# Kernel optimization log

Measured on AMD Instinct MI355X. Metric: run time of the kernel, lower is better.

Reference implementation:

```python
import jax, jax.numpy as jnp
import numpy as np

B, T, C, H = 4, 2048, 1024, 16
D = C // H  # head dim = 64


def setup_inputs() -> dict:
    key = jax.random.key(0)
    ks = jax.random.split(key, 5)
    s = 1.0 / np.sqrt(C)
    return {
        "x": jax.random.normal(ks[0], (B, T, C), dtype=jnp.float32),
        "Wq": jax.random.normal(ks[1], (C, C), dtype=jnp.float32) * s,
        "bq": jnp.zeros((C,), dtype=jnp.float32),
        "Wk": jax.random.normal(ks[2], (C, C), dtype=jnp.float32) * s,
        "bk": jnp.zeros((C,), dtype=jnp.float32),
        "Wv": jax.random.normal(ks[3], (C, C), dtype=jnp.float32) * s,
        "bv": jnp.zeros((C,), dtype=jnp.float32),
        "Wp": jax.random.normal(ks[4], (C, C), dtype=jnp.float32) * s,
        "bp": jnp.zeros((C,), dtype=jnp.float32),
    }


def reference(x, Wq, bq, Wk, bk, Wv, bv, Wp, bp):
    Bb, Tt, Cc = x.shape
    # QKV projections (torch Linear: y = x @ W.T + b)
    q = (x @ Wq.T + bq).reshape(Bb, Tt, H, D).transpose(0, 2, 1, 3)  # [B,H,T,D]
    k = (x @ Wk.T + bk).reshape(Bb, Tt, H, D).transpose(0, 2, 1, 3)
    v = (x @ Wv.T + bv).reshape(Bb, Tt, H, D).transpose(0, 2, 1, 3)
    att = jnp.einsum("bhqd,bhkd->bhqk", q, k) / jnp.sqrt(jnp.float32(D))
    causal = jnp.tril(jnp.ones((Tt, Tt), dtype=bool))
    att = jnp.where(causal[None, None], att, -jnp.inf)
    att = jax.nn.softmax(att, axis=-1)
    y = jnp.einsum("bhqk,bhkd->bhqd", att, v)  # [B,H,T,D]
    y = y.transpose(0, 2, 1, 3).reshape(Bb, Tt, Cc)
    return y @ Wp.T + bp
```

## Files before the change

### kernel.cpp

```cpp
#include <hip/hip_runtime.h>

typedef unsigned short u16;
typedef unsigned int u32;

typedef __attribute__((ext_vector_type(4))) float f32x4;
typedef __attribute__((ext_vector_type(8))) short bf16x8;


__device__ inline u16 f2b(float f) {
  union { float f; u32 u; } x; x.f = f;
  u32 u = x.u;
  u32 r = (u + 0x7fffu + ((u >> 16) & 1u)) >> 16;
  return (u16)r;
}

__device__ inline u32 cvtpk(float lo, float hi) {
  u32 r;
  asm("v_cvt_pk_bf16_f32 %0, %1, %2" : "=v"(r) : "v"(lo), "v"(hi));
  return r;
}

__device__ inline void gload_lds16(const void* g, void* l) {
  __builtin_amdgcn_global_load_lds(
      (const __attribute__((address_space(1))) u32*)g,
      (__attribute__((address_space(3))) u32*)l, 16, 0, 0);
}


__global__ __launch_bounds__(256) void cvt_all(const float* __restrict__ x,
                                               const float* __restrict__ w0,
                                               const float* __restrict__ w1,
                                               const float* __restrict__ w2,
                                               const float* __restrict__ w3,
                                               u16* __restrict__ xs,
                                               u16* __restrict__ wsz,
                                               u16* __restrict__ wps) {
  int g = blockIdx.x * 256 + threadIdx.x;
  int grow = g >> 7;
  int c = g & 127;
  const float* src;
  char* dst;
  int row;
  if (grow < 8192) {
    row = grow;
    src = x + (size_t)row * 1024;
    dst = (char*)xs;
  } else if (grow < 11264) {
    row = grow - 8192;
    src = (row < 1024) ? w0 + (size_t)row * 1024
         : (row < 2048) ? w1 + (size_t)(row - 1024) * 1024
                        : w2 + (size_t)(row - 2048) * 1024;
    dst = (char*)wsz;
  } else {
    row = grow - 11264;
    src = w3 + (size_t)row * 1024;
    dst = (char*)wps;
  }
  int kt = c >> 3, cc = (c & 7) ^ (row & 7);
  float4 lo = *(const float4*)(src + c * 8);
  float4 hi = *(const float4*)(src + c * 8 + 4);
  union { u16 s[8]; uint4 v; } o;
  o.s[0] = f2b(lo.x); o.s[1] = f2b(lo.y); o.s[2] = f2b(lo.z); o.s[3] = f2b(lo.w);
  o.s[4] = f2b(hi.x); o.s[5] = f2b(hi.y); o.s[6] = f2b(hi.z); o.s[7] = f2b(hi.w);
  *(uint4*)(dst + (size_t)(row >> 8) * 524288 + kt * 32768 +
            (row & 255) * 128 + cc * 16) = o.v;
}


__global__ __launch_bounds__(512) void gemm_qkv(const u16* __restrict__ Aswz,
                                                const u16* __restrict__ Wswz,
                                                const float* __restrict__ bq,
                                                const float* __restrict__ bk,
                                                const float* __restrict__ bv,
                                                u16* __restrict__ outQ,
                                                u16* __restrict__ outK,
                                                u16* __restrict__ outVt,
                                                float qscale) {
  __shared__ u16 lds[3][24576];

  const int t = threadIdx.x;
  const int lane = t & 63;
  const int w = t >> 6;
  const int wm = w >> 1, wn = w & 1;
  const int lr = lane & 15, lg = lane >> 4;

  int bid = blockIdx.y * 24 + blockIdx.x;
  int swz = (bid & 7) * 96 + (bid >> 3);
  const int mBase = (swz / 24) * 256;
  const int nBase = (swz % 24) * 128;
  const int mode = nBase >> 10;
  const int noff = nBase & 255;

  const char* Ap = (const char*)Aswz + (size_t)(mBase >> 8) * 524288;
  const char* Bp = (const char*)Wswz + (size_t)(nBase >> 8) * 524288 +
                   noff * 128;

  f32x4 acc[4][4];
#pragma unroll
  for (int i = 0; i < 4; ++i)
#pragma unroll
    for (int j = 0; j < 4; ++j) acc[i][j] = (f32x4){0.f, 0.f, 0.f, 0.f};

  auto stage = [&](int buf, int kt2) {
    const char* As = Ap + (size_t)kt2 * 32768;
    const char* Bs = Bp + (size_t)kt2 * 32768;
    char* Ad = (char*)&lds[buf][0];
    char* Bd = (char*)&lds[buf][16384];
#pragma unroll
    for (int l = 0; l < 4; ++l)
      gload_lds16(As + (l * 512 + t) * 16, Ad + (l * 512 + t) * 16);
#pragma unroll
    for (int l = 0; l < 2; ++l)
      gload_lds16(Bs + (l * 512 + t) * 16, Bd + (l * 512 + t) * 16);
  };

  stage(0, 0);
  stage(1, 1);

  for (int kt = 0; kt < 16; ++kt) {
    if (kt < 15) asm volatile("s_waitcnt vmcnt(6)" ::: "memory");
    else         asm volatile("s_waitcnt vmcnt(0)" ::: "memory");
    __builtin_amdgcn_s_barrier();
    if (kt + 2 < 16) stage((kt + 2) % 3, kt + 2);

    const int cb = kt % 3;
    const char* Ab = (const char*)&lds[cb][0];
    const char* Bb = (const char*)&lds[cb][16384];

    bf16x8 af[4][2], bf[4][2];
#pragma unroll
    for (int i = 0; i < 4; ++i) {
      int row = wm * 64 + i * 16 + lr;
#pragma unroll
      for (int kk = 0; kk < 2; ++kk)
        af[i][kk] = *(const bf16x8*)(Ab + row * 128 +
                                     ((kk * 64 + lg * 16) ^ ((row & 7) << 4)));
    }
#pragma unroll
    for (int j = 0; j < 4; ++j) {
      int rn = wn * 64 + j * 16 + lr;
#pragma unroll
      for (int kk = 0; kk < 2; ++kk)
        bf[j][kk] = *(const bf16x8*)(Bb + rn * 128 +
                                     ((kk * 64 + lg * 16) ^ ((rn & 7) << 4)));
    }

    __builtin_amdgcn_s_setprio(1);
#pragma unroll
    for (int i = 0; i < 4; ++i)
#pragma unroll
      for (int j = 0; j < 4; ++j)
#pragma unroll
        for (int kk = 0; kk < 2; ++kk)
          acc[i][j] = __builtin_amdgcn_mfma_f32_16x16x32_bf16(
              af[i][kk], bf[j][kk], acc[i][j], 0, 0, 0);
    __builtin_amdgcn_s_setprio(0);
  }

#pragma unroll
  for (int i = 0; i < 4; ++i) {
    int row = mBase + wm * 64 + i * 16 + lg * 4;
    int b_ = row >> 11, tp = row & 2047;
#pragma unroll
    for (int j = 0; j < 4; ++j) {
      int col = nBase + wn * 64 + j * 16 + lr;
      int ncol = col & 1023;
      int h = ncol >> 6, dd = ncol & 63;
      size_t bhOff = (size_t)(b_ * 16 + h) * 262144;
      if (mode == 2) {
        float bv_ = bv[ncol];
        ushort4 o;
        o.x = f2b(acc[i][j][0] + bv_);
        o.y = f2b(acc[i][j][1] + bv_);
        o.z = f2b(acc[i][j][2] + bv_);
        o.w = f2b(acc[i][j][3] + bv_);
        *(ushort4*)((char*)outVt + bhOff + (tp >> 6) * 8192 + dd * 128 +
                    ((((tp & 63) >> 3) << 4) ^ ((dd & 7) << 4)) +
                    (tp & 7) * 2) = o;
      } else if (mode == 0) {
        float bv_ = bq[ncol];
#pragma unroll
        for (int r = 0; r < 4; ++r)
          outQ[(((size_t)(b_ * 16 + h) * 2048) + tp + r) * 64 + dd] =
              f2b((acc[i][j][r] + bv_) * qscale);
      } else {
        float bv_ = bk[ncol];
#pragma unroll
        for (int r = 0; r < 4; ++r) {
          int tt = tp + r;
          *(u16*)((char*)outK + bhOff + (tt >> 6) * 8192 + (tt & 63) * 128 +
                  (((dd >> 3) << 4) ^ ((tt & 7) << 4)) + (dd & 7) * 2) =
              f2b(acc[i][j][r] + bv_);
        }
      }
    }
  }
}


__global__ __launch_bounds__(512) void gemm_proj(const u16* __restrict__ Aswz,
                                                 const u16* __restrict__ Wswz,
                                                 const float* __restrict__ bias,
                                                 float* __restrict__ outF) {
  __shared__ u16 lds[3][24576];

  const int t = threadIdx.x;
  const int lane = t & 63;
  const int w = t >> 6;
  const int wm = w >> 1, wn = w & 1;
  const int lr = lane & 15, lg = lane >> 4;

  int bid = blockIdx.y * 8 + blockIdx.x;
  int swz = (bid & 7) * 32 + (bid >> 3);
  const int mBase = (swz >> 3) * 256;
  const int nBase = (swz & 7) * 128;

  const char* Ap = (const char*)Aswz + (size_t)(mBase >> 8) * 524288;
  const char* Bp = (const char*)Wswz + (size_t)(nBase >> 8) * 524288 +
                   (nBase & 255) * 128;

  f32x4 acc[4][4];
#pragma unroll
  for (int i = 0; i < 4; ++i)
#pragma unroll
    for (int j = 0; j < 4; ++j) acc[i][j] = (f32x4){0.f, 0.f, 0.f, 0.f};

  auto stage = [&](int buf, int kt2) {
    const char* As = Ap + (size_t)kt2 * 32768;
    const char* Bs = Bp + (size_t)kt2 * 32768;
    char* Ad = (char*)&lds[buf][0];
    char* Bd = (char*)&lds[buf][16384];
#pragma unroll
    for (int l = 0; l < 4; ++l)
      gload_lds16(As + (l * 512 + t) * 16, Ad + (l * 512 + t) * 16);
#pragma unroll
    for (int l = 0; l < 2; ++l)
      gload_lds16(Bs + (l * 512 + t) * 16, Bd + (l * 512 + t) * 16);
  };

  stage(0, 0);
  stage(1, 1);

  for (int kt = 0; kt < 16; ++kt) {
    if (kt < 15) asm volatile("s_waitcnt vmcnt(6)" ::: "memory");
    else         asm volatile("s_waitcnt vmcnt(0)" ::: "memory");
    __builtin_amdgcn_s_barrier();
    if (kt + 2 < 16) stage((kt + 2) % 3, kt + 2);

    const int cb = kt % 3;
    const char* Ab = (const char*)&lds[cb][0];
    const char* Bb = (const char*)&lds[cb][16384];

    bf16x8 af[4][2], bf[4][2];
#pragma unroll
    for (int i = 0; i < 4; ++i) {
      int row = wm * 64 + i * 16 + lr;
#pragma unroll
      for (int kk = 0; kk < 2; ++kk)
        af[i][kk] = *(const bf16x8*)(Ab + row * 128 +
                                     ((kk * 64 + lg * 16) ^ ((row & 7) << 4)));
    }
#pragma unroll
    for (int j = 0; j < 4; ++j) {
      int rn = wn * 64 + j * 16 + lr;
#pragma unroll
      for (int kk = 0; kk < 2; ++kk)
        bf[j][kk] = *(const bf16x8*)(Bb + rn * 128 +
                                     ((kk * 64 + lg * 16) ^ ((rn & 7) << 4)));
    }

    __builtin_amdgcn_s_setprio(1);
#pragma unroll
    for (int i = 0; i < 4; ++i)
#pragma unroll
      for (int j = 0; j < 4; ++j)
#pragma unroll
        for (int kk = 0; kk < 2; ++kk)
          acc[i][j] = __builtin_amdgcn_mfma_f32_16x16x32_bf16(
              af[i][kk], bf[j][kk], acc[i][j], 0, 0, 0);
    __builtin_amdgcn_s_setprio(0);
  }

#pragma unroll
  for (int i = 0; i < 4; ++i) {
    int row = mBase + wm * 64 + i * 16 + lg * 4;
#pragma unroll
    for (int j = 0; j < 4; ++j) {
      int col = nBase + wn * 64 + j * 16 + lr;
      float bv = bias[col];
#pragma unroll
      for (int r = 0; r < 4; ++r)
        outF[(size_t)(row + r) * 1024 + col] = acc[i][j][r] + bv;
    }
  }
}


__global__ __launch_bounds__(512) void attn_fwd(const u16* __restrict__ qg,
                                                const u16* __restrict__ kswz,
                                                const u16* __restrict__ vswz,
                                                u16* __restrict__ ypan) {
  __shared__ u16 sK[2][64 * 64];
  __shared__ u16 sVt[2][64 * 64];

  const int t = threadIdx.x;
  const int lane = t & 63;
  const int w = t >> 6;
  const int lr = lane & 15, lg = lane >> 4;
  const int xk = (lr & 7) << 4;

  int bid0 = blockIdx.y * 8 + blockIdx.x;
  int swzb = (bid0 & 7) * 64 + (bid0 >> 3);
  const int bh = swzb >> 3;
  const int pair = swzb & 7;

  const char* kgb = (const char*)kswz + (size_t)bh * 262144;
  const char* vgb = (const char*)vswz + (size_t)bh * 262144;
  const u16* qb = qg + (size_t)bh * 131072;

  gload_lds16(kgb + t * 16, (char*)&sK[0][0] + t * 16);
  gload_lds16(vgb + t * 16, (char*)&sVt[0][0] + t * 16);

  f32x4 zero = {0.f, 0.f, 0.f, 0.f};
  const int b = bh >> 4, h = bh & 15;
  int tc = 0;

  for (int half = 0; half < 2; ++half) {
    const int qt = half ? pair : 15 - pair;
    const int nkt = 2 * qt + 2;
    const int wq0 = qt * 128 + w * 16;
    const int qrow = wq0 + lr;

    bf16x8 qf[2];
#pragma unroll
    for (int kk = 0; kk < 2; ++kk)
      qf[kk] = *(const bf16x8*)(qb + (size_t)qrow * 64 + kk * 32 + lg * 8);

    f32x4 accO[4];
#pragma unroll
    for (int n = 0; n < 4; ++n) accO[n] = zero;
    float lrun = 0.f;

    for (int kt = 0; kt < nkt; ++kt, ++tc) {
      const int cur = tc & 1;
      __syncthreads();

      int nextT = (kt + 1 < nkt) ? kt + 1 : (half == 0 ? 0 : -1);
      if (nextT >= 0) {
        gload_lds16(kgb + nextT * 8192 + t * 16,
                    (char*)&sK[cur ^ 1][0] + t * 16);
        gload_lds16(vgb + nextT * 8192 + t * 16,
                    (char*)&sVt[cur ^ 1][0] + t * 16);
      }

      if (kt * 64 > wq0 + 15) continue;

      const char* kb_ = (const char*)&sK[cur][0];
      const char* vb_ = (const char*)&sVt[cur][0];

      f32x4 s[4];
      __builtin_amdgcn_s_setprio(1);
#pragma unroll
      for (int n = 0; n < 4; ++n) {
        f32x4 a = zero;
#pragma unroll
        for (int kk = 0; kk < 2; ++kk) {
          bf16x8 kf = *(const bf16x8*)(kb_ + (n * 16 + lr) * 128 +
                                       ((kk * 64 + lg * 16) ^ xk));
          a = __builtin_amdgcn_mfma_f32_16x16x32_bf16(kf, qf[kk], a, 0, 0, 0);
        }
        s[n] = a;
      }
      __builtin_amdgcn_s_setprio(0);

      if (kt * 64 + 63 > wq0) {
#pragma unroll
        for (int n = 0; n < 4; ++n) {
          int key0 = kt * 64 + n * 16 + lg * 4;
#pragma unroll
          for (int r = 0; r < 4; ++r)
            s[n][r] = (key0 + r <= qrow) ? s[n][r] : -1e30f;
        }
      }

      u32 pk[4][2];
#pragma unroll
      for (int n = 0; n < 4; ++n) {
        float p0 = exp2f(s[n][0] - 12.f);
        float p1 = exp2f(s[n][1] - 12.f);
        float p2 = exp2f(s[n][2] - 12.f);
        float p3 = exp2f(s[n][3] - 12.f);
        lrun += (p0 + p1) + (p2 + p3);
        pk[n][0] = cvtpk(p0, p1);
        pk[n][1] = cvtpk(p2, p3);
      }

      const bool hi = (lg >> 1) & 1;
#pragma unroll
      for (int kk = 0; kk < 2; ++kk) {
        u32 g[4];
#pragma unroll
        for (int r = 0; r < 4; ++r) {
          const int rh = r >> 1, rl = r & 1;
          u32 give = ((lg & 1) ^ rh) ? pk[2 * kk + 1][rl] : pk[2 * kk][rl];
          int srcLane = ((lg & 1) * 2 + ((lg >> 1) ^ rh)) * 16 + lr;
          g[r] = (u32)__shfl((int)give, srcLane);
        }
        union { u32 u[4]; bf16x8 v; } pu;
        pu.u[0] = hi ? g[2] : g[0];
        pu.u[1] = hi ? g[3] : g[1];
        pu.u[2] = hi ? g[0] : g[2];
        pu.u[3] = hi ? g[1] : g[3];
        bf16x8 pf = pu.v;
        __builtin_amdgcn_s_setprio(1);
#pragma unroll
        for (int n = 0; n < 4; ++n) {
          bf16x8 vf = *(const bf16x8*)(vb_ + (n * 16 + lr) * 128 +
                                       ((kk * 64 + lg * 16) ^ xk));
          accO[n] = __builtin_amdgcn_mfma_f32_16x16x32_bf16(pf, vf, accO[n], 0, 0, 0);
        }
        __builtin_amdgcn_s_setprio(0);
      }
    }

    lrun += __shfl_xor(lrun, 16);
    lrun += __shfl_xor(lrun, 32);

#pragma unroll
    for (int r = 0; r < 4; ++r) {
      float linv = 1.f / __shfl(lrun, lg * 4 + r);
      int row = b * 2048 + qt * 128 + w * 16 + lg * 4 + r;
      char* rp = (char*)ypan + (size_t)(row >> 8) * 524288 +
                 h * 32768 + (row & 255) * 128;
#pragma unroll
      for (int n = 0; n < 4; ++n) {
        int cl = n * 16 + lr;
        *(u16*)(rp + ((((cl >> 3) ^ (row & 7)) << 4)) + (cl & 7) * 2) =
            f2b(accO[n][r] * linv);
      }
    }
  }
}


extern "C" void kernel_launch(void* const* d_in, const int* in_sizes, int n_in,
                              void* d_out, int out_size, void* d_ws, size_t ws_size,
                              hipStream_t stream) {
  const float* x  = (const float*)d_in[0];
  const float* Wq = (const float*)d_in[1];
  const float* bq = (const float*)d_in[2];
  const float* Wk = (const float*)d_in[3];
  const float* bk = (const float*)d_in[4];
  const float* Wv = (const float*)d_in[5];
  const float* bv = (const float*)d_in[6];
  const float* Wp = (const float*)d_in[7];
  const float* bp = (const float*)d_in[8];
  float* out = (float*)d_out;

  char* ws = (char*)d_ws;
  u16* xb  = (u16*)(ws);
  u16* wqb = (u16*)(ws + (16u << 20));
  u16* wpb = (u16*)(ws + (22u << 20));
  u16* qb  = (u16*)(ws + (24u << 20));
  u16* kb  = (u16*)(ws + (40u << 20));
  u16* vtb = (u16*)(ws + (56u << 20));
  u16* yb  = (u16*)(ws + (72u << 20));

  const float SCL = 0.18033688011112042f;

  cvt_all<<<6144, 256, 0, stream>>>(x, Wq, Wk, Wv, Wp, xb, wqb, wpb);

  gemm_qkv<<<dim3(24, 32), 512, 0, stream>>>(xb, wqb, bq, bk, bv,
                                             qb, kb, vtb, SCL);

  attn_fwd<<<dim3(8, 64), 512, 0, stream>>>(qb, kb, vtb, yb);

  gemm_proj<<<dim3(8, 32), 512, 0, stream>>>(yb, wpb, bp, out);
}
```

Baseline: 175.9 us.

## Use 32x32 MFMA tiles and split paired query tiles across wave halves

The attention kernel switches from 16x16x32 to 32x32x16 bf16 MFMAs, so each wave handles 32 query rows instead of 16. The two paired query tiles now run concurrently, with waves 0-3 on the long tile and waves 4-7 on the short one, instead of one after the other. This reduces loop iterations, barriers and K/V reloads. The cost is that the short-tile waves sit idle through the later key tiles, accumulator register use grows, and the softmax permutation is redone with a single xor-32 shuffle.

```diff
diff --git a/kernel.cpp b/kernel.cpp
--- a/kernel.cpp
+++ b/kernel.cpp
@@ -4,6 +4,7 @@
 typedef unsigned int u32;
 
 typedef __attribute__((ext_vector_type(4))) float f32x4;
+typedef __attribute__((ext_vector_type(16))) float f32x16;
 typedef __attribute__((ext_vector_type(8))) short bf16x8;
 
 
@@ -306,8 +307,8 @@
   const int t = threadIdx.x;
   const int lane = t & 63;
   const int w = t >> 6;
-  const int lr = lane & 15, lg = lane >> 4;
-  const int xk = (lr & 7) << 4;
+  const int qc = lane & 31;
+  const int hi = lane >> 5;
 
   int bid0 = blockIdx.y * 8 + blockIdx.x;
   int swzb = (bid0 & 7) * 64 + (bid0 >> 3);
@@ -318,126 +319,125 @@
   const char* vgb = (const char*)vswz + (size_t)bh * 262144;
   const u16* qb = qg + (size_t)bh * 131072;
 
+  const int qt = (w < 4) ? (15 - pair) : pair;
+  const int wq0 = qt * 128 + (w & 3) * 32;
+  const int qrow = wq0 + qc;
+  const int nkt = 2 * (15 - pair) + 2;
+
+  bf16x8 qf[4];
+#pragma unroll
+  for (int s = 0; s < 4; ++s)
+    qf[s] = *(const bf16x8*)(qb + (size_t)qrow * 64 + s * 16 + hi * 8);
+
   gload_lds16(kgb + t * 16, (char*)&sK[0][0] + t * 16);
   gload_lds16(vgb + t * 16, (char*)&sVt[0][0] + t * 16);
 
-  f32x4 zero = {0.f, 0.f, 0.f, 0.f};
+  f32x16 accO[2];
+#pragma unroll
+  for (int d = 0; d < 2; ++d)
+#pragma unroll
+    for (int i = 0; i < 16; ++i) accO[d][i] = 0.f;
+  float lrun = 0.f;
+
   const int b = bh >> 4, h = bh & 15;
-  int tc = 0;
-
-  for (int half = 0; half < 2; ++half) {
-    const int qt = half ? pair : 15 - pair;
-    const int nkt = 2 * qt + 2;
-    const int wq0 = qt * 128 + w * 16;
-    const int qrow = wq0 + lr;
-
-    bf16x8 qf[2];
-#pragma unroll
-    for (int kk = 0; kk < 2; ++kk)
-      qf[kk] = *(const bf16x8*)(qb + (size_t)qrow * 64 + kk * 32 + lg * 8);
-
-    f32x4 accO[4];
-#pragma unroll
-    for (int n = 0; n < 4; ++n) accO[n] = zero;
-    float lrun = 0.f;
-
-    for (int kt = 0; kt < nkt; ++kt, ++tc) {
-      const int cur = tc & 1;
-      __syncthreads();
-
-      int nextT = (kt + 1 < nkt) ? kt + 1 : (half == 0 ? 0 : -1);
-      if (nextT >= 0) {
-        gload_lds16(kgb + nextT * 8192 + t * 16,
-                    (char*)&sK[cur ^ 1][0] + t * 16);
-        gload_lds16(vgb + nextT * 8192 + t * 16,
-                    (char*)&sVt[cur ^ 1][0] + t * 16);
+
+  for (int kt = 0; kt < nkt; ++kt) {
+    const int cur = kt & 1;
+    __syncthreads();
+
+    if (kt + 1 < nkt) {
+      gload_lds16(kgb + (kt + 1) * 8192 + t * 16,
+                  (char*)&sK[cur ^ 1][0] + t * 16);
+      gload_lds16(vgb + (kt + 1) * 8192 + t * 16,
+                  (char*)&sVt[cur ^ 1][0] + t * 16);
+    }
+
+    if (kt * 64 > wq0 + 31) continue;
+
+    const char* kb_ = (const char*)&sK[cur][0];
+    const char* vb_ = (const char*)&sVt[cur][0];
+
+    f32x16 sb[2];
+    __builtin_amdgcn_s_setprio(1);
+#pragma unroll
+    for (int n = 0; n < 2; ++n) {
+      f32x16 a;
+#pragma unroll
+      for (int i = 0; i < 16; ++i) a[i] = 0.f;
+      const int key = n * 32 + qc;
+#pragma unroll
+      for (int s = 0; s < 4; ++s) {
+        bf16x8 kf = *(const bf16x8*)(kb_ + key * 128 +
+                                     ((s * 32 + hi * 16) ^ ((key & 7) << 4)));
+        a = __builtin_amdgcn_mfma_f32_32x32x16_bf16(kf, qf[s], a, 0, 0, 0);
       }
-
-      if (kt * 64 > wq0 + 15) continue;
-
-      const char* kb_ = (const char*)&sK[cur][0];
-      const char* vb_ = (const char*)&sVt[cur][0];
-
-      f32x4 s[4];
+      sb[n] = a;
+    }
+    __builtin_amdgcn_s_setprio(0);
+
+    if (kt * 64 + 63 > wq0) {
+#pragma unroll
+      for (int n = 0; n < 2; ++n)
+#pragma unroll
+        for (int r = 0; r < 16; ++r) {
+          int key = kt * 64 + n * 32 + (r & 3) + 8 * (r >> 2) + 4 * hi;
+          sb[n][r] = (key <= qrow) ? sb[n][r] : -1e30f;
+        }
+    }
+
+#pragma unroll
+    for (int n = 0; n < 2; ++n)
+#pragma unroll
+      for (int r = 0; r < 16; ++r) {
+        float v = exp2f(sb[n][r] - 12.f);
+        lrun += v;
+        sb[n][r] = v;
+      }
+
+#pragma unroll
+    for (int s = 0; s < 4; ++s) {
+      const int n = s >> 1;
+      const int o0 = (s & 1) * 2, o1 = o0 + 1;
+      u32 p00 = cvtpk(sb[n][4 * o0 + 0], sb[n][4 * o0 + 1]);
+      u32 p01 = cvtpk(sb[n][4 * o0 + 2], sb[n][4 * o0 + 3]);
+      u32 p10 = cvtpk(sb[n][4 * o1 + 0], sb[n][4 * o1 + 1]);
+      u32 p11 = cvtpk(sb[n][4 * o1 + 2], sb[n][4 * o1 + 3]);
+      u32 a0 = hi ? p10 : p00, a1 = hi ? p11 : p01;
+      u32 b0 = hi ? p00 : p10, b1 = hi ? p01 : p11;
+      u32 r0 = (u32)__shfl_xor((int)b0, 32);
+      u32 r1 = (u32)__shfl_xor((int)b1, 32);
+      union { u32 u[4]; bf16x8 v; } pu;
+      pu.u[0] = hi ? r0 : a0;
+      pu.u[1] = hi ? r1 : a1;
+      pu.u[2] = hi ? a0 : r0;
+      pu.u[3] = hi ? a1 : r1;
       __builtin_amdgcn_s_setprio(1);
 #pragma unroll
-      for (int n = 0; n < 4; ++n) {
-        f32x4 a = zero;
-#pragma unroll
-        for (int kk = 0; kk < 2; ++kk) {
-          bf16x8 kf = *(const bf16x8*)(kb_ + (n * 16 + lr) * 128 +
-                                       ((kk * 64 + lg * 16) ^ xk));
-          a = __builtin_amdgcn_mfma_f32_16x16x32_bf16(kf, qf[kk], a, 0, 0, 0);
-        }
-        s[n] = a;
+      for (int db = 0; db < 2; ++db) {
+        const int d = db * 32 + qc;
+        bf16x8 vf = *(const bf16x8*)(vb_ + d * 128 +
+                                     ((s * 32 + hi * 16) ^ ((d & 7) << 4)));
+        accO[db] = __builtin_amdgcn_mfma_f32_32x32x16_bf16(pu.v, vf,
+                                                           accO[db], 0, 0, 0);
       }
       __builtin_amdgcn_s_setprio(0);
-
-      if (kt * 64 + 63 > wq0) {
-#pragma unroll
-        for (int n = 0; n < 4; ++n) {
-          int key0 = kt * 64 + n * 16 + lg * 4;
-#pragma unroll
-          for (int r = 0; r < 4; ++r)
-            s[n][r] = (key0 + r <= qrow) ? s[n][r] : -1e30f;
-        }
-      }
-
-      u32 pk[4][2];
-#pragma unroll
-      for (int n = 0; n < 4; ++n) {
-        float p0 = exp2f(s[n][0] - 12.f);
-        float p1 = exp2f(s[n][1] - 12.f);
-        float p2 = exp2f(s[n][2] - 12.f);
-        float p3 = exp2f(s[n][3] - 12.f);
-        lrun += (p0 + p1) + (p2 + p3);
-        pk[n][0] = cvtpk(p0, p1);
-        pk[n][1] = cvtpk(p2, p3);
-      }
-
-      const bool hi = (lg >> 1) & 1;
-#pragma unroll
-      for (int kk = 0; kk < 2; ++kk) {
-        u32 g[4];
-#pragma unroll
-        for (int r = 0; r < 4; ++r) {
-          const int rh = r >> 1, rl = r & 1;
-          u32 give = ((lg & 1) ^ rh) ? pk[2 * kk + 1][rl] : pk[2 * kk][rl];
-          int srcLane = ((lg & 1) * 2 + ((lg >> 1) ^ rh)) * 16 + lr;
-          g[r] = (u32)__shfl((int)give, srcLane);
-        }
-        union { u32 u[4]; bf16x8 v; } pu;
-        pu.u[0] = hi ? g[2] : g[0];
-        pu.u[1] = hi ? g[3] : g[1];
-        pu.u[2] = hi ? g[0] : g[2];
-        pu.u[3] = hi ? g[1] : g[3];
-        bf16x8 pf = pu.v;
-        __builtin_amdgcn_s_setprio(1);
-#pragma unroll
-        for (int n = 0; n < 4; ++n) {
-          bf16x8 vf = *(const bf16x8*)(vb_ + (n * 16 + lr) * 128 +
-                                       ((kk * 64 + lg * 16) ^ xk));
-          accO[n] = __builtin_amdgcn_mfma_f32_16x16x32_bf16(pf, vf, accO[n], 0, 0, 0);
-        }
-        __builtin_amdgcn_s_setprio(0);
-      }
-    }
-
-    lrun += __shfl_xor(lrun, 16);
-    lrun += __shfl_xor(lrun, 32);
-
-#pragma unroll
-    for (int r = 0; r < 4; ++r) {
-      float linv = 1.f / __shfl(lrun, lg * 4 + r);
-      int row = b * 2048 + qt * 128 + w * 16 + lg * 4 + r;
-      char* rp = (char*)ypan + (size_t)(row >> 8) * 524288 +
-                 h * 32768 + (row & 255) * 128;
-#pragma unroll
-      for (int n = 0; n < 4; ++n) {
-        int cl = n * 16 + lr;
-        *(u16*)(rp + ((((cl >> 3) ^ (row & 7)) << 4)) + (cl & 7) * 2) =
-            f2b(accO[n][r] * linv);
-      }
+    }
+  }
+
+  lrun += __shfl_xor(lrun, 32);
+
+#pragma unroll
+  for (int r = 0; r < 16; ++r) {
+    const int q_r = (r & 3) + 8 * (r >> 2) + 4 * hi;
+    float linv = 1.f / __shfl(lrun, q_r);
+    int row = b * 2048 + wq0 + q_r;
+    char* rp = (char*)ypan + (size_t)(row >> 8) * 524288 +
+               h * 32768 + (row & 255) * 128;
+#pragma unroll
+    for (int db = 0; db < 2; ++db) {
+      int cl = db * 32 + qc;
+      *(u16*)(rp + (((cl >> 3) ^ (row & 7)) << 4) + (cl & 7) * 2) =
+          f2b(accO[db][r] * linv);
     }
   }
 }
```

Result: slower. 179.9 us (+2.3%).
